# Optimization experiments

Hardware: AMD Instinct MI355X
Metric: run time of the kernel (lower is better)

Reference implementation:

```python
import jax, jax.numpy as jnp
import numpy as np

K = 16  # hardcoded in the torch module (reshape([-1, 16]))


def setup_inputs() -> dict:
    key = jax.random.key(0)
    B, M = 32, 2048
    N = B * M
    ks = jax.random.split(key, 7)
    pos = jax.random.normal(ks[0], (N, 3), dtype=jnp.float32)
    batch = jnp.repeat(jnp.arange(B, dtype=jnp.int32), M)  # sorted, equal-size graphs

    def lin(k_, fi, fo):
        lim = 1.0 / np.sqrt(fi)
        w = jax.random.uniform(k_, (fi, fo), jnp.float32, -lim, lim)
        b = jax.random.uniform(jax.random.fold_in(k_, 1), (fo,), jnp.float32, -lim, lim)
        return w, b

    W1, b1 = lin(ks[1], K * 6, 1024)
    W2, b2 = lin(ks[2], 1024, 256)
    W3, b3 = lin(ks[3], 256, 9)
    return {"pos": pos, "batch": batch, "num_graphs": B,
            "W1": W1, "b1": b1, "W2": W2, "b2": b2, "W3": W3, "b3": b3}


def _knn_idx(pos, num_graphs):
    # equal-size graphs laid out contiguously -> batched brute-force knn
    N = pos.shape[0]
    M = N // num_graphs
    p = pos.reshape(num_graphs, M, 3)
    sq = jnp.sum(p * p, axis=-1)                      # [B, M]
    # squared distances [B, M, M]; self-distance ~0 so loop=True self-edge is kept
    d2 = sq[:, :, None] + sq[:, None, :] - 2.0 * jnp.einsum('bid,bjd->bij', p, p)
    _, idx = jax.lax.top_k(-d2, K)                    # [B, M, K] local indices
    offs = (jnp.arange(num_graphs, dtype=idx.dtype) * M)[:, None, None]
    return (idx + offs).reshape(N, K)                 # global neighbour indices


def reference(pos, batch, num_graphs, W1, b1, W2, b2, W3, b3):
    N = pos.shape[0]
    M = N // num_graphs
    nbr_idx = _knn_idx(pos, num_graphs)               # [N, K]
    neighbours = pos[nbr_idx]                         # [N, K, 3] gather
    center = pos[:, None, :]                          # [N, 1, 3]
    feat = jnp.concatenate(
        [jnp.broadcast_to(center, (N, K, 3)), center - neighbours], axis=2
    ).reshape(N, K * 6)                               # [N, 96]
    h = jax.nn.relu(feat @ W1 + b1)
    h = jax.nn.relu(h @ W2 + b2)
    x9 = h @ W3 + b3                                  # [N, 9]
    pooled = x9.reshape(num_graphs, M, 9).mean(axis=1)  # global_mean_pool -> [B, 9]
    T = pooled[batch].reshape(N, 3, 3)                # gather back per node
    return jnp.einsum('nd,ndk->nk', pos, T)           # bmm([N,1,3],[N,3,3]) squeezed
```

## Files before the change

kernel.cpp:

```cpp
#include <hip/hip_runtime.h>
#include <stdint.h>

#define NPTS   65536
#define MPTS   2048
#define NGRAPH 32

typedef short s16x8 __attribute__((ext_vector_type(8)));
typedef float f32x4 __attribute__((ext_vector_type(4)));

#define FEATP_OFF 0u
#define W1P_OFF   12582912u
#define W2P_OFF   12779520u
#define SACC_OFF  13303808u
#define POOLT_OFF 13336576u
#define ZKEY_OFF  13337728u

#define PAD  128
#define ZN   (MPTS + 2 * PAD)

__device__ __forceinline__ unsigned short f2bf(float f) {
  unsigned u = __float_as_uint(f);
  u = (u + 0x7FFFu + ((u >> 16) & 1u)) >> 16;
  return (unsigned short)u;
}

__device__ __forceinline__ void ce32(unsigned& a, unsigned& b) {
  unsigned lo = __builtin_elementwise_min(a, b);
  b = __builtin_elementwise_max(a, b);
  a = lo;
}

template <int N>
__device__ __forceinline__ void sortN(unsigned* k) {
#pragma unroll
  for (int p = 1; p < N; p <<= 1)
#pragma unroll
    for (int q = p; q >= 1; q >>= 1)
#pragma unroll
      for (int j = q % p; j + q < N; j += 2 * q)
#pragma unroll
        for (int i = 0; i < q; ++i)
          if (i + j + q < N)
            if ((i + j) / (2 * p) == (i + j + q) / (2 * p))
              ce32(k[i + j], k[i + j + q]);
}

__device__ __forceinline__ void mergelow8(unsigned r[8], const unsigned b[8]) {
#pragma unroll
  for (int i = 0; i < 8; ++i)
    r[i] = __builtin_elementwise_min(r[i], b[7 - i]);
#pragma unroll
  for (int d = 4; d >= 1; d >>= 1)
#pragma unroll
    for (int i = 0; i < 8; ++i)
      if ((i & d) == 0) ce32(r[i], r[i + d]);
}

__device__ __forceinline__ void mergelow16(unsigned r[16], const unsigned b[16]) {
#pragma unroll
  for (int i = 0; i < 16; ++i)
    r[i] = __builtin_elementwise_min(r[i], b[15 - i]);
#pragma unroll
  for (int d = 8; d >= 1; d >>= 1)
#pragma unroll
    for (int i = 0; i < 16; ++i)
      if ((i & d) == 0) ce32(r[i], r[i + d]);
}

__global__ __launch_bounds__(512) void prep(
    const float* __restrict__ pos, const float* __restrict__ W1,
    const float* __restrict__ W2, unsigned* __restrict__ zkeysG,
    unsigned short* __restrict__ w1p, unsigned short* __restrict__ w2p,
    float* __restrict__ sacc)
{
  __shared__ unsigned sk[MPTS];
  int b = blockIdx.x;
  int tid = threadIdx.x;
  if (b < NGRAPH) {
    const float* gp = pos + (size_t)b * MPTS * 3;
    int w = tid >> 6, l = tid & 63;
    unsigned v[4];
#pragma unroll
    for (int s = 0; s < 4; ++s) {
      int i = w * 256 + s * 64 + l;
      unsigned u = __float_as_uint(gp[i * 3 + 2]);
      u ^= ((unsigned)(((int)u) >> 31)) | 0x80000000u;
      v[s] = (u & 0xFFFFF800u) | (unsigned)i;
    }
#pragma unroll
    for (int kk = 1; kk <= 11; ++kk) {
      const int k2 = 1 << kk;
      if (k2 >= 512) {
        __syncthreads();
#pragma unroll
        for (int s = 0; s < 4; ++s) sk[w * 256 + s * 64 + l] = v[s];
#pragma unroll
        for (int j = k2 >> 1; j >= 256; j >>= 1) {
          __syncthreads();
#pragma unroll
          for (int e = 0; e < 4; ++e) {
            int i = tid + (e << 9);
            int ix = i ^ j;
            if (ix > i) {
              unsigned a = sk[i], b2 = sk[ix];
              bool up = ((i & k2) == 0);
              unsigned lo = __builtin_elementwise_min(a, b2);
              unsigned hi = __builtin_elementwise_max(a, b2);
              sk[i] = up ? lo : hi;
              sk[ix] = up ? hi : lo;
            }
          }
        }
        __syncthreads();
#pragma unroll
        for (int s = 0; s < 4; ++s) v[s] = sk[w * 256 + s * 64 + l];
      }
#pragma unroll
      for (int j = 128; j >= 64; j >>= 1) {
        if (k2 > j) {
          int sd = j >> 6;
#pragma unroll
          for (int s = 0; s < 4; ++s) {
            int sp = s ^ sd;
            if (sp > s) {
              bool up = (((w * 256 + s * 64 + l) & k2) == 0);
              unsigned lo = __builtin_elementwise_min(v[s], v[sp]);
              unsigned hi = __builtin_elementwise_max(v[s], v[sp]);
              v[s] = up ? lo : hi;
              v[sp] = up ? hi : lo;
            }
          }
        }
      }
#pragma unroll
      for (int j = 32; j >= 1; j >>= 1) {
        if (k2 > j) {
#pragma unroll
          for (int s = 0; s < 4; ++s) {
            unsigned p = __shfl_xor(v[s], j, 64);
            bool up = (((w * 256 + s * 64 + l) & k2) == 0);
            bool lower = ((l & j) == 0);
            v[s] = (lower == up) ? __builtin_elementwise_min(v[s], p)
                                 : __builtin_elementwise_max(v[s], p);
          }
        }
      }
    }
#pragma unroll
    for (int s = 0; s < 4; ++s)
      zkeysG[(b << 11) + w * 256 + s * 64 + l] = v[s];
  } else {
    int pid = (b - NGRAPH) * 512 + tid;
    if (pid < 98304) {
      int k = pid >> 10, n = pid & 1023;
      int kt = k >> 5, h = (k >> 3) & 3, j = k & 7;
      int nt = n >> 4, cc = n & 15;
      w1p[((size_t)(kt * 64 + nt) * 64 + h * 16 + cc) * 8 + j] = f2bf(W1[pid]);
    } else if (pid < 98304 + 262144) {
      int t = pid - 98304;
      int k = t >> 8, n = t & 255;
      int kt = k >> 5, h = (k >> 3) & 3, j = k & 7;
      int nt = n >> 4, cc = n & 15;
      w2p[((size_t)(kt * 16 + nt) * 64 + h * 16 + cc) * 8 + j] = f2bf(W2[t]);
    } else if (pid < 360448 + 8192) {
      sacc[pid - 360448] = 0.0f;
    }
  }
}

__global__ __launch_bounds__(512, 4) void knn_feat(
    const float* __restrict__ pos, const unsigned* __restrict__ zkeysG,
    unsigned short* __restrict__ featp)
{
  __shared__ float4 zq[ZN];
  const float INF = __uint_as_float(0x7F800000u);
  int g = blockIdx.x >> 5;
  const float* gp = pos + (size_t)g * MPTS * 3;
  for (int i = threadIdx.x; i < ZN; i += 512) {
    float4 v;
    if (i < PAD) v = make_float4(INF, INF, -INF, INF);
    else if (i >= MPTS + PAD) v = make_float4(INF, INF, INF, INF);
    else {
      int o = (int)(zkeysG[(g << 11) + (i - PAD)] & 0x7FFu);
      float x = gp[o * 3], y = gp[o * 3 + 1], z = gp[o * 3 + 2];
      v = make_float4(x, y, z, fmaf(x, x, fmaf(y, y, z * z)));
    }
    zq[i] = v;
  }
  __syncthreads();

  int l = threadIdx.x & 63, w = threadIdx.x >> 6;
  int qv = l & 7, t = l >> 3;
  int R0 = ((w << 5) | (blockIdx.x & 31)) << 3;
  int R = R0 + qv;
  float4 c = zq[R + PAD];
  float cs = c.w, cz = c.z;
  float zc = 0.5f * (zq[R0 + PAD].z + zq[R0 + PAD + 7].z);

  unsigned run[8];
#pragma unroll
  for (int i = 0; i < 8; ++i) run[i] = 0xFFFFFFFFu;
  unsigned B = 0xFFFFFFFFu;

  int LO = R0 + PAD, HI = R0 + PAD;
  float zl = zq[LO - 1].z, zr = zq[HI].z;

  for (int step = 0; step < 18; ++step) {
    bool canL = (LO >= PAD), canR = (HI + PAD <= ZN);
    unsigned thr = (B > 0xFFFEFFFFu) ? 0xFFFFFFFFu : B + 0x10000u;
    float dl = cz - zl, dr = zr - cz;
    bool doneL = !canL || ((__float_as_uint(dl * dl) & 0xFFFFF800u) > thr);
    bool doneR = !canR || ((__float_as_uint(dr * dr) & 0xFFFFF800u) > thr);
    if (__all(doneL && doneR)) break;

    bool goR = canR && (!canL || ((zr - zc) <= (zc - zl)));
    int base = goR ? HI : LO - PAD;
    if (goR) HI += PAD; else LO -= PAD;

    zl = (LO >= 1) ? zq[LO - 1].z : -INF;
    zr = (HI < ZN) ? zq[HI].z : INF;

    int bt = base + t;
    unsigned k[16];
#pragma unroll
    for (int i = 0; i < 16; ++i) {
      int p = bt + (i << 3);
      float4 P = zq[p];
      float dot = fmaf(c.x, P.x, fmaf(c.y, P.y, c.z * P.z));
      float d2 = fmaf(-2.0f, dot, cs + P.w);
      k[i] = (__float_as_uint(d2) & 0xFFFFF800u) |
             ((unsigned)(p - PAD) & 0x7FFu);
    }
    sortN<8>(k); sortN<8>(k + 8);
    mergelow8(k, k + 8);
    mergelow8(run, k);

    unsigned bb = run[1];
    bb = __builtin_elementwise_max(bb, (unsigned)__shfl_xor(bb, 8, 64));
    bb = __builtin_elementwise_max(bb, (unsigned)__shfl_xor(bb, 16, 64));
    bb = __builtin_elementwise_max(bb, (unsigned)__shfl_xor(bb, 32, 64));
    B = bb;
  }

  unsigned t16[16];
  {
    unsigned oth[8];
#pragma unroll
    for (int i = 0; i < 8; ++i) oth[i] = __shfl_xor(run[i], 8, 64);
#pragma unroll
    for (int i = 0; i < 8; ++i) {
      unsigned a = run[i], x = oth[7 - i];
      t16[i]     = __builtin_elementwise_min(a, x);
      t16[i + 8] = __builtin_elementwise_max(a, x);
    }
#pragma unroll
    for (int d = 4; d >= 1; d >>= 1)
#pragma unroll
      for (int i = 0; i < 16; ++i)
        if ((i & d) == 0) ce32(t16[i], t16[i + d]);
  }
#pragma unroll
  for (int m = 16; m <= 32; m <<= 1) {
    unsigned o2[16];
#pragma unroll
    for (int i = 0; i < 16; ++i) o2[i] = __shfl_xor(t16[i], m, 64);
    mergelow16(t16, o2);
  }

  if (t == 0) {
    float nx[16], ny[16], nz[16];
#pragma unroll
    for (int i = 0; i < 16; ++i) {
      int rk = (int)(t16[i] & 0x7FFu);
      float4 p = zq[rk + PAD];
      nx[i] = p.x; ny[i] = p.y; nz[i] = p.z;
    }
    int n = g * MPTS + R;
    unsigned short* op = featp + (size_t)(n >> 4) * 1536 + (size_t)(n & 15) * 8;
#pragma unroll
    for (int kt = 0; kt < 3; ++kt) {
#pragma unroll
      for (int h = 0; h < 4; ++h) {
        s16x8 v;
#pragma unroll
        for (int j = 0; j < 8; ++j) {
          int f = kt * 32 + h * 8 + j;
          int kn = f / 6, comp = f % 6;
          float val;
          if      (comp == 0) val = c.x;
          else if (comp == 1) val = c.y;
          else if (comp == 2) val = c.z;
          else if (comp == 3) val = c.x - nx[kn];
          else if (comp == 4) val = c.y - ny[kn];
          else                val = c.z - nz[kn];
          v[j] = (short)f2bf(val);
        }
        *(s16x8*)(op + kt * 512 + h * 128) = v;
      }
    }
  }
}

__global__ __launch_bounds__(512, 2) void mlp_fused(
    const unsigned short* __restrict__ featp,
    const unsigned short* __restrict__ w1p,
    const unsigned short* __restrict__ w2p,
    const float* __restrict__ b1, const float* __restrict__ b2,
    float* __restrict__ sacc)
{
  __shared__ unsigned short h1c[2][64][136];

  int tid = threadIdx.x;
  int w = tid >> 6, lane = tid & 63;
  int b = blockIdx.x;
  int g = b >> 5;
  int ks = lane >> 4;
  int cl = lane & 15;

  s16x8 a1[4][3];
#pragma unroll
  for (int m = 0; m < 4; ++m) {
    const unsigned short* ap = featp + (size_t)(b * 4 + m) * 1536 + (size_t)lane * 8;
#pragma unroll
    for (int kt = 0; kt < 3; ++kt) a1[m][kt] = *(const s16x8*)(ap + kt * 512);
  }

  f32x4 acc2[4][2];
#pragma unroll
  for (int m = 0; m < 4; ++m) {
    acc2[m][0] = (f32x4){0, 0, 0, 0};
    acc2[m][1] = (f32x4){0, 0, 0, 0};
  }

  s16x8 b1f[3];
#pragma unroll
  for (int kt = 0; kt < 3; ++kt)
    b1f[kt] = *(const s16x8*)(w1p + ((size_t)(kt * 64 + w) * 64 + lane) * 8);

  for (int c = 0; c < 8; ++c) {
    int buf = c & 1;
    s16x8 b2f[8];
#pragma unroll
    for (int kt2 = 0; kt2 < 4; ++kt2)
#pragma unroll
      for (int j = 0; j < 2; ++j)
        b2f[kt2 * 2 + j] = *(const s16x8*)(
            w2p + ((size_t)((c * 4 + kt2) * 16 + (w * 2 + j)) * 64 + lane) * 8);

    float bias1 = b1[(c * 8 + w) * 16 + cl];
#pragma unroll
    for (int m = 0; m < 4; ++m) {
      f32x4 acc1 = (f32x4){0, 0, 0, 0};
#pragma unroll
      for (int kt = 0; kt < 3; ++kt)
        acc1 = __builtin_amdgcn_mfma_f32_16x16x32_bf16(a1[m][kt], b1f[kt], acc1, 0, 0, 0);
#pragma unroll
      for (int r = 0; r < 4; ++r) {
        float v = acc1[r] + bias1;
        v = v > 0.0f ? v : 0.0f;
        h1c[buf][m * 16 + ks * 4 + r][w * 16 + cl] = f2bf(v);
      }
    }

    if (c < 7) {
#pragma unroll
      for (int kt = 0; kt < 3; ++kt)
        b1f[kt] = *(const s16x8*)(
            w1p + ((size_t)(kt * 64 + (c + 1) * 8 + w) * 64 + lane) * 8);
    }
    __syncthreads();

#pragma unroll
    for (int kt2 = 0; kt2 < 4; ++kt2) {
      s16x8 afr[4];
#pragma unroll
      for (int m = 0; m < 4; ++m)
        afr[m] = *(const s16x8*)&h1c[buf][m * 16 + cl][kt2 * 32 + ks * 8];
#pragma unroll
      for (int j = 0; j < 2; ++j)
#pragma unroll
        for (int m = 0; m < 4; ++m)
          acc2[m][j] = __builtin_amdgcn_mfma_f32_16x16x32_bf16(
              afr[m], b2f[kt2 * 2 + j], acc2[m][j], 0, 0, 0);
    }
  }

  float sj0 = 0.0f, sj1 = 0.0f;
  {
    float bias20 = b2[(2 * w + 0) * 16 + cl];
    float bias21 = b2[(2 * w + 1) * 16 + cl];
#pragma unroll
    for (int m = 0; m < 4; ++m)
#pragma unroll
      for (int r = 0; r < 4; ++r) {
        float v0 = acc2[m][0][r] + bias20;
        float v1 = acc2[m][1][r] + bias21;
        sj0 += v0 > 0.0f ? v0 : 0.0f;
        sj1 += v1 > 0.0f ? v1 : 0.0f;
      }
  }
#pragma unroll
  for (int m = 16; m <= 32; m <<= 1) {
    sj0 += __shfl_xor(sj0, m, 64);
    sj1 += __shfl_xor(sj1, m, 64);
  }
  if (ks == 0) {
    atomicAdd(&sacc[g * 256 + (2 * w + 0) * 16 + cl], sj0);
    atomicAdd(&sacc[g * 256 + (2 * w + 1) * 16 + cl], sj1);
  }
}

__global__ __launch_bounds__(96) void pool_w3(
    const float* __restrict__ sacc, const float* __restrict__ W3,
    const float* __restrict__ b3, float* __restrict__ pooledT)
{
  int gid = blockIdx.x * 96 + threadIdx.x;
  if (gid >= NGRAPH * 9) return;
  int g = gid / 9, o = gid % 9;
  float acc = 0.0f;
  const float* sp = sacc + g * 256;
#pragma unroll 8
  for (int k = 0; k < 256; ++k) acc = fmaf(sp[k], W3[k * 9 + o], acc);
  pooledT[gid] = fmaf(acc, 1.0f / (float)MPTS, b3[o]);
}

__global__ __launch_bounds__(256) void finalize(
    const float* __restrict__ pos, const int* __restrict__ batch,
    const float* __restrict__ pooledT, float* __restrict__ out)
{
  int n = blockIdx.x * 256 + threadIdx.x;
  if (n >= NPTS) return;
  int bb = batch[n];
  float px = pos[n * 3], py = pos[n * 3 + 1], pz = pos[n * 3 + 2];
  const float* P = pooledT + bb * 9;
#pragma unroll
  for (int k2 = 0; k2 < 3; ++k2)
    out[n * 3 + k2] = fmaf(px, P[k2], fmaf(py, P[3 + k2], pz * P[6 + k2]));
}

extern "C" void kernel_launch(void* const* d_in, const int* in_sizes, int n_in,
                              void* d_out, int out_size, void* d_ws, size_t ws_size,
                              hipStream_t stream) {
  const float* pos  = (const float*)d_in[0];
  const int*   batch = (const int*)d_in[1];
  const float* W1 = (const float*)d_in[3];
  const float* b1 = (const float*)d_in[4];
  const float* W2 = (const float*)d_in[5];
  const float* b2 = (const float*)d_in[6];
  const float* W3 = (const float*)d_in[7];
  const float* b3 = (const float*)d_in[8];

  char* ws = (char*)d_ws;
  unsigned short* featp = (unsigned short*)(ws + FEATP_OFF);
  unsigned short* w1p   = (unsigned short*)(ws + W1P_OFF);
  unsigned short* w2p   = (unsigned short*)(ws + W2P_OFF);
  float*          sacc  = (float*)(ws + SACC_OFF);
  float*          pooledT = (float*)(ws + POOLT_OFF);
  unsigned*       zkeysG = (unsigned*)(ws + ZKEY_OFF);
  float*          out = (float*)d_out;

  prep<<<dim3(752), dim3(512), 0, stream>>>(pos, W1, W2, zkeysG, w1p, w2p, sacc);
  knn_feat<<<dim3(1024), dim3(512), 0, stream>>>(pos, zkeysG, featp);
  mlp_fused<<<dim3(1024), dim3(512), 0, stream>>>(featp, w1p, w2p, b1, b2, sacc);
  pool_w3<<<dim3(3), dim3(96), 0, stream>>>(sacc, W3, b3, pooledT);
  finalize<<<dim3(256), dim3(256), 0, stream>>>(pos, batch, pooledT, out);
}
```

Baseline: 127.9 us.

## Skip kNN merge when no candidate improves; software-pipeline W2 loads in MLP

In the kNN scan, each wave first computes the minimum candidate key and skips the sort/merge and threshold update when no lane has a candidate below its current 8th-best. This removes sorting work for windows that cannot improve the result. In the fused MLP, the chunk loop is unrolled by two with double-buffered W2 fragment registers, so the next chunk's W2 loads are issued before the current GEMM2 runs. Layer-1 biases are also preloaded. The cost is more register pressure under launch_bounds(512,2), plus an extra reduction and a wave vote on every kNN iteration.

New measurement: 135.5 us. +5.9%, slower.

```diff
diff --git a/kernel.cpp b/kernel.cpp
--- a/kernel.cpp
+++ b/kernel.cpp
@@ -231,15 +231,21 @@
       k[i] = (__float_as_uint(d2) & 0xFFFFF800u) |
              ((unsigned)(p - PAD) & 0x7FFu);
     }
-    sortN<8>(k); sortN<8>(k + 8);
-    mergelow8(k, k + 8);
-    mergelow8(run, k);
-
-    unsigned bb = run[1];
-    bb = __builtin_elementwise_max(bb, (unsigned)__shfl_xor(bb, 8, 64));
-    bb = __builtin_elementwise_max(bb, (unsigned)__shfl_xor(bb, 16, 64));
-    bb = __builtin_elementwise_max(bb, (unsigned)__shfl_xor(bb, 32, 64));
-    B = bb;
+
+    unsigned vmin = k[0];
+#pragma unroll
+    for (int i = 1; i < 16; ++i) vmin = __builtin_elementwise_min(vmin, k[i]);
+    if (__any(vmin < run[7])) {
+      sortN<8>(k); sortN<8>(k + 8);
+      mergelow8(k, k + 8);
+      mergelow8(run, k);
+
+      unsigned bb = run[1];
+      bb = __builtin_elementwise_max(bb, (unsigned)__shfl_xor(bb, 8, 64));
+      bb = __builtin_elementwise_max(bb, (unsigned)__shfl_xor(bb, 16, 64));
+      bb = __builtin_elementwise_max(bb, (unsigned)__shfl_xor(bb, 32, 64));
+      B = bb;
+    }
   }
 
   unsigned t16[16];
@@ -301,6 +307,58 @@
   }
 }
 
+__device__ __forceinline__ void load_b1(s16x8 (&dst)[3],
+    const unsigned short* __restrict__ w1p, int nt, int lane) {
+#pragma unroll
+  for (int kt = 0; kt < 3; ++kt)
+    dst[kt] = *(const s16x8*)(w1p + ((size_t)(kt * 64 + nt) * 64 + lane) * 8);
+}
+
+__device__ __forceinline__ void load_b2(s16x8 (&dst)[8],
+    const unsigned short* __restrict__ w2p, int c, int w, int lane) {
+#pragma unroll
+  for (int kt2 = 0; kt2 < 4; ++kt2)
+#pragma unroll
+    for (int j = 0; j < 2; ++j)
+      dst[kt2 * 2 + j] = *(const s16x8*)(
+          w2p + ((size_t)((c * 4 + kt2) * 16 + (w * 2 + j)) * 64 + lane) * 8);
+}
+
+__device__ __forceinline__ void gemm1_step(const s16x8 (&a1)[4][3],
+    const s16x8 (&b1f)[3], float bias1,
+    unsigned short (*h1buf)[136], int w, int cl, int ks) {
+#pragma unroll
+  for (int m = 0; m < 4; ++m) {
+    f32x4 acc1 = (f32x4){0, 0, 0, 0};
+#pragma unroll
+    for (int kt = 0; kt < 3; ++kt)
+      acc1 = __builtin_amdgcn_mfma_f32_16x16x32_bf16(a1[m][kt], b1f[kt], acc1, 0, 0, 0);
+#pragma unroll
+    for (int r = 0; r < 4; ++r) {
+      float v = acc1[r] + bias1;
+      v = v > 0.0f ? v : 0.0f;
+      h1buf[m * 16 + ks * 4 + r][w * 16 + cl] = f2bf(v);
+    }
+  }
+}
+
+__device__ __forceinline__ void gemm2_step(const s16x8 (&b2f)[8],
+    f32x4 (&acc2)[4][2], const unsigned short (*h1buf)[136], int cl, int ks) {
+#pragma unroll
+  for (int kt2 = 0; kt2 < 4; ++kt2) {
+    s16x8 afr[4];
+#pragma unroll
+    for (int m = 0; m < 4; ++m)
+      afr[m] = *(const s16x8*)&h1buf[m * 16 + cl][kt2 * 32 + ks * 8];
+#pragma unroll
+    for (int j = 0; j < 2; ++j)
+#pragma unroll
+      for (int m = 0; m < 4; ++m)
+        acc2[m][j] = __builtin_amdgcn_mfma_f32_16x16x32_bf16(
+            afr[m], b2f[kt2 * 2 + j], acc2[m][j], 0, 0, 0);
+  }
+}
+
 __global__ __launch_bounds__(512, 2) void mlp_fused(
     const unsigned short* __restrict__ featp,
     const unsigned short* __restrict__ w1p,
@@ -332,57 +390,28 @@
     acc2[m][1] = (f32x4){0, 0, 0, 0};
   }
 
+  float bias1v[8];
+#pragma unroll
+  for (int c = 0; c < 8; ++c) bias1v[c] = b1[(c * 8 + w) * 16 + cl];
+
   s16x8 b1f[3];
-#pragma unroll
-  for (int kt = 0; kt < 3; ++kt)
-    b1f[kt] = *(const s16x8*)(w1p + ((size_t)(kt * 64 + w) * 64 + lane) * 8);
-
-  for (int c = 0; c < 8; ++c) {
-    int buf = c & 1;
-    s16x8 b2f[8];
-#pragma unroll
-    for (int kt2 = 0; kt2 < 4; ++kt2)
-#pragma unroll
-      for (int j = 0; j < 2; ++j)
-        b2f[kt2 * 2 + j] = *(const s16x8*)(
-            w2p + ((size_t)((c * 4 + kt2) * 16 + (w * 2 + j)) * 64 + lane) * 8);
-
-    float bias1 = b1[(c * 8 + w) * 16 + cl];
-#pragma unroll
-    for (int m = 0; m < 4; ++m) {
-      f32x4 acc1 = (f32x4){0, 0, 0, 0};
-#pragma unroll
-      for (int kt = 0; kt < 3; ++kt)
-        acc1 = __builtin_amdgcn_mfma_f32_16x16x32_bf16(a1[m][kt], b1f[kt], acc1, 0, 0, 0);
-#pragma unroll
-      for (int r = 0; r < 4; ++r) {
-        float v = acc1[r] + bias1;
-        v = v > 0.0f ? v : 0.0f;
-        h1c[buf][m * 16 + ks * 4 + r][w * 16 + cl] = f2bf(v);
-      }
-    }
-
-    if (c < 7) {
-#pragma unroll
-      for (int kt = 0; kt < 3; ++kt)
-        b1f[kt] = *(const s16x8*)(
-            w1p + ((size_t)(kt * 64 + (c + 1) * 8 + w) * 64 + lane) * 8);
-    }
+  load_b1(b1f, w1p, w, lane);
+  s16x8 b2a[8], b2b[8];
+  load_b2(b2a, w2p, 0, w, lane);
+
+#pragma unroll
+  for (int cc = 0; cc < 8; cc += 2) {
+    gemm1_step(a1, b1f, bias1v[cc], h1c[0], w, cl, ks);
+    load_b1(b1f, w1p, (cc + 1) * 8 + w, lane);
     __syncthreads();
-
-#pragma unroll
-    for (int kt2 = 0; kt2 < 4; ++kt2) {
-      s16x8 afr[4];
-#pragma unroll
-      for (int m = 0; m < 4; ++m)
-        afr[m] = *(const s16x8*)&h1c[buf][m * 16 + cl][kt2 * 32 + ks * 8];
-#pragma unroll
-      for (int j = 0; j < 2; ++j)
-#pragma unroll
-        for (int m = 0; m < 4; ++m)
-          acc2[m][j] = __builtin_amdgcn_mfma_f32_16x16x32_bf16(
-              afr[m], b2f[kt2 * 2 + j], acc2[m][j], 0, 0, 0);
-    }
+    load_b2(b2b, w2p, cc + 1, w, lane);
+    gemm2_step(b2a, acc2, h1c[0], cl, ks);
+
+    gemm1_step(a1, b1f, bias1v[cc + 1], h1c[1], w, cl, ks);
+    if (cc + 2 < 8) load_b1(b1f, w1p, (cc + 2) * 8 + w, lane);
+    __syncthreads();
+    if (cc + 2 < 8) load_b2(b2a, w2p, cc + 2, w, lane);
+    gemm2_step(b2b, acc2, h1c[1], cl, ks);
   }
 
   float sj0 = 0.0f, sj1 = 0.0f;
```
